# Performance work log

Measured on AMD Instinct MI355X. Metric: run time of the kernel, lower is better.

The kernel has to match this reference:

```python
import jax, jax.numpy as jnp
import numpy as np

B = 2
DZ, DY, DX = 10, 200, 176
N_PER = 100000                      # active voxels per batch element
C_IN, C_MID, C_OUT = 64, 32, 64
STRIDE = 8

_OFFS = np.stack(np.meshgrid(np.arange(3), np.arange(3), np.arange(3), indexing='ij'), -1).reshape(27, 3)


def _build_indices():
    rng = np.random.RandomState(0)
    rows = []
    for b in range(B):
        lin = rng.choice(DZ * DY * DX, size=N_PER, replace=False)
        z, y, x = np.unravel_index(lin, (DZ, DY, DX))
        rows.append(np.stack([np.full(N_PER, b), z, y, x], 1))
    return np.concatenate(rows, 0).astype(np.int32)


def _neighbor_maps(indices):
    # spconv-style indice generation (pure integer bookkeeping, done once in numpy)
    N = indices.shape[0]
    OZ, OY, OX = (DZ - 1) // 2 + 1, (DY - 1) // 2 + 1, (DX - 1) // 2 + 1  # k3 s2 p1 output shape
    hi = np.array([OZ, OY, OX])
    hin = np.array([DZ, DY, DX])
    i3 = indices[:, 1:4].astype(np.int64)
    cand = i3[:, None, :] + 1 - _OFFS[None]          # o*stride = i + pad - k
    valid = (cand % 2 == 0).all(-1)
    o3 = cand // 2
    valid &= ((o3 >= 0) & (o3 < hi)).all(-1)
    ob = np.broadcast_to(indices[:, 0:1], (N, 27))
    flat = np.stack([ob[valid], o3[..., 0][valid], o3[..., 1][valid], o3[..., 2][valid]], 1)
    down = np.unique(flat, axis=0).astype(np.int32)  # [M,4] stride-2 conv output coords
    M = down.shape[0]
    in_grid = -np.ones((B, DZ, DY, DX), np.int32)
    in_grid[indices[:, 0], indices[:, 1], indices[:, 2], indices[:, 3]] = np.arange(N)
    dn_grid = -np.ones((B, OZ, OY, OX), np.int32)
    dn_grid[down[:, 0], down[:, 1], down[:, 2], down[:, 3]] = np.arange(M)
    # stride-2 conv: output row m, kernel k <- input at o*2 - 1 + k
    src = down[:, None, 1:4].astype(np.int64) * 2 - 1 + _OFFS[None]
    ok = ((src >= 0) & (src < hin)).all(-1)
    srcc = np.clip(src, 0, hin - 1)
    nbr_down = np.where(ok, in_grid[down[:, 0:1], srcc[..., 0], srcc[..., 1], srcc[..., 2]], -1).astype(np.int32)
    # submanifold 3x3x3 on down coords
    d3 = down[:, None, 1:4].astype(np.int64) + (_OFFS[None] - 1)
    ok2 = ((d3 >= 0) & (d3 < hi)).all(-1)
    d3c = np.clip(d3, 0, hi - 1)
    nbr_sub = np.where(ok2, dn_grid[down[:, 0:1], d3c[..., 0], d3c[..., 1], d3c[..., 2]], -1).astype(np.int32)
    # inverse conv (transposed pairs of the stride-2 conv): input row n, kernel k <- down row at (i+1-k)/2
    o3c = np.clip(o3, 0, hi - 1)
    nbr_inv = np.where(valid, dn_grid[indices[:, 0:1], o3c[..., 0], o3c[..., 1], o3c[..., 2]], -1).astype(np.int32)
    return down, nbr_down, nbr_sub, nbr_inv


def setup_inputs():
    key = jax.random.key(0)
    ks = jax.random.split(key, 12)
    indices = _build_indices()
    down_indices, nbr_down, nbr_sub, nbr_inv = _neighbor_maps(indices)
    N = indices.shape[0]
    w = lambda k, shp: jax.random.normal(k, shp, jnp.float32) * 0.05
    l2r = np.array([[0., -1., 0., 0.], [0., 0., -1., 0.], [1., 0., 0., 0.]], np.float32)  # lidar->rect
    p2 = np.array([[721.54, 0., 609.56, 44.85], [0., 721.54, 172.85, 0.216], [0., 0., 1., 0.0027]], np.float32)
    return {
        'features': jax.random.normal(ks[0], (N, C_IN), jnp.float32),
        'W_down1': w(ks[1], (27, C_IN, C_MID)),
        'W_res': w(ks[2], (27, C_IN, C_MID)),
        'W_sub2': w(ks[3], (27, C_MID, C_MID)),
        'W_2d1': w(ks[4], (9, C_MID, C_MID)),
        'W_2d2': w(ks[5], (9, C_MID, C_MID)),
        'W_sub3': w(ks[6], (27, C_MID, C_MID)),
        'W_inv4': w(ks[7], (27, C_MID, C_OUT)),
        'bn32_g': 1.0 + 0.1 * jax.random.normal(ks[8], (7, C_MID), jnp.float32),
        'bn32_b': 0.1 * jax.random.normal(ks[9], (7, C_MID), jnp.float32),
        'bn64_g': 1.0 + 0.1 * jax.random.normal(ks[10], (2, C_OUT), jnp.float32),
        'bn64_b': 0.1 * jax.random.normal(ks[11], (2, C_OUT), jnp.float32),
        'calib_l2r': jnp.asarray(np.tile(l2r, (B, 1, 1))),
        'calib_p2': jnp.asarray(np.tile(p2, (B, 1, 1))),
        'down_indices': jnp.asarray(down_indices),
        'nbr_down': jnp.asarray(nbr_down),
        'nbr_sub': jnp.asarray(nbr_sub),
        'nbr_inv': jnp.asarray(nbr_inv),
        'stride': STRIDE,
        'batch_size': B,
    }


def _bn(x, g, b, eps=1e-3):
    # BatchNorm1d training-mode forward (batch stats, biased variance, eps=1e-3)
    m = x.mean(0)
    v = x.var(0)
    return (x - m) * jax.lax.rsqrt(v + eps) * g + b


def _gconv(feats, nbr, W):
    # spconv gather -> GEMM -> accumulate; nbr[m,k] is source row or -1
    out = jnp.zeros((nbr.shape[0], W.shape[-1]), feats.dtype)
    for k in range(W.shape[0]):
        idx = nbr[:, k]
        m = (idx >= 0).astype(feats.dtype)[:, None]
        out = out + (feats[jnp.maximum(idx, 0)] * m) @ W[k]
    return out


def _index2uv(down_indices, calib_l2r, calib_p2, stride):
    vs = 0.05 * stride
    fi = down_indices.astype(jnp.float32)
    x = fi[:, 3] * vs + (0.0 + vs / 2)
    y = fi[:, 2] * vs + (-40.0 + vs / 2)
    z = fi[:, 1] * vs + (-3.0 + vs / 2)
    pts = jnp.stack([x, y, z, jnp.ones_like(x)], 1)           # [M,4] homogeneous lidar pts
    b = down_indices[:, 0]
    rect = jnp.einsum('mi,mji->mj', pts, calib_l2r[b])        # lidar_to_rect
    rh = jnp.concatenate([rect, jnp.ones_like(rect[:, :1])], 1)
    proj = jnp.einsum('mi,mji->mj', rh, calib_p2[b])          # rect_to_img
    u = jax.lax.stop_gradient(proj[:, 0] / proj[:, 2]).astype(jnp.int32)
    v = jax.lax.stop_gradient(proj[:, 1] / proj[:, 2]).astype(jnp.int32)
    u = jnp.clip(u, 0, 1400 - stride) // stride
    v = jnp.clip(v, 0, 400 - stride) // stride
    return b, u, v


def reference(features, W_down1, W_res, W_sub2, W_2d1, W_2d2, W_sub3, W_inv4,
              bn32_g, bn32_b, bn64_g, bn64_b, calib_l2r, calib_p2,
              down_indices, nbr_down, nbr_sub, nbr_inv, stride, batch_size):
    relu = jax.nn.relu
    d3 = relu(_bn(_gconv(features, nbr_down, W_down1), bn32_g[0], bn32_b[0]))   # d3_conv1 (spconv s2)
    d3 = relu(_bn(_gconv(d3, nbr_sub, W_sub2), bn32_g[1], bn32_b[1]))           # d3_conv2 (subm)
    res = relu(_bn(_gconv(features, nbr_down, W_res), bn32_g[2], bn32_b[2]))    # resnet_layer (spconv s2)
    d3 = d3 + res
    # 3D -> 2D reprojection (index2uv) and 2D submanifold conv stage
    b, u, v = _index2uv(down_indices, calib_l2r, calib_p2, stride)
    U, V = 1400 // stride, 400 // stride
    M = d3.shape[0]
    grid = -jnp.ones((batch_size, U, V), jnp.int32)
    grid = grid.at[b, u, v].max(jnp.arange(M, dtype=jnp.int32))  # deterministic dedupe of uv collisions
    du = jnp.repeat(jnp.arange(-1, 2), 3)
    dv = jnp.tile(jnp.arange(-1, 2), 3)
    uu = u[:, None] + du[None]
    vv = v[:, None] + dv[None]
    ok = (uu >= 0) & (uu < U) & (vv >= 0) & (vv < V)
    nbr2d = jnp.where(ok, grid[b[:, None], jnp.clip(uu, 0, U - 1), jnp.clip(vv, 0, V - 1)], -1)
    d2 = relu(_bn(_gconv(d3, nbr2d, W_2d1), bn32_g[3], bn32_b[3]))              # d2_conv1
    d2 = relu(_bn(_gconv(d2, nbr2d, W_2d2), bn32_g[4], bn32_b[4]))              # d2_conv2
    d3 = _bn(d3 + d2, bn32_g[5], bn32_b[5])                                     # mid_norm_fn (no relu)
    d3 = relu(_bn(_gconv(d3, nbr_sub, W_sub3), bn32_g[6], bn32_b[6]))           # d3_conv3
    out = relu(_bn(_gconv(d3, nbr_inv, W_inv4), bn64_g[0], bn64_b[0]))          # d3_conv4 (inverse conv)
    out = _bn(out + features, bn64_g[1], bn64_b[1])                             # output_norm_fn
    return out
```

## Files before the change

### kernel.cpp

```cpp
#include <hip/hip_runtime.h>

#define NBANK 64
#define ACC_STRIDE (NBANK * 128)

typedef _Float16 half8 __attribute__((ext_vector_type(8)));
typedef float    fx4   __attribute__((ext_vector_type(4)));

__global__ void init_kernel(float* __restrict__ acc, int accN, _Float16* __restrict__ zrow,
                            int* __restrict__ grid, int gridN)
{
    int i = blockIdx.x * 256 + threadIdx.x;
    if (i < accN) acc[i] = 0.f;
    if (i < 64) ((float*)zrow)[i] = 0.f;
    if (i < gridN) grid[i] = -1;
}

struct WDesc { const float* W; _Float16* H; _Float16* L; int K, CIN, COUT, base; };
struct WArgs { WDesc d[7]; int total; };

__global__ void wsplit_all_kernel(WArgs a)
{
    int t = blockIdx.x * 256 + threadIdx.x;
    if (t >= a.total) return;
    int seg = 0;
    #pragma unroll
    for (int s = 1; s < 7; ++s) if (t >= a.d[s].base) seg = s;
    const WDesc D = a.d[seg];
    int tt   = t - D.base;
    int lane = tt & 63;
    int frag = tt >> 6;
    int NT = D.COUT >> 4, NS = D.CIN >> 5;
    int ct = frag % NT;
    int s2 = (frag / NT) % NS;
    int k  = frag / (NT * NS);
    int col = ct * 16 + (lane & 15);
    int cib = s2 * 32 + ((lane >> 4) << 3);
    half8 vh, vl;
    #pragma unroll
    for (int j = 0; j < 8; ++j) {
        float w = D.W[(size_t)(k * D.CIN + cib + j) * D.COUT + col];
        _Float16 hh = (_Float16)w;
        vh[j] = hh;
        vl[j] = (_Float16)(w - (float)hh);
    }
    *(half8*)(D.H + (size_t)tt * 8) = vh;
    *(half8*)(D.L + (size_t)tt * 8) = vl;
}

__global__ void tof16_kernel(const float* __restrict__ x, _Float16* __restrict__ h, long total)
{
    long base = ((long)blockIdx.x * 256 + threadIdx.x) * 8;
    if (base >= total) return;
    fx4 v0 = *(const fx4*)(x + base);
    fx4 v1 = *(const fx4*)(x + base + 4);
    half8 hh;
    #pragma unroll
    for (int j = 0; j < 4; ++j) { hh[j] = (_Float16)v0[j]; hh[4 + j] = (_Float16)v1[j]; }
    *(half8*)(h + base) = hh;
}

template <int CIN, int COUT, int K, bool DUAL>
__global__ __launch_bounds__(256) void gconv_mfma_kernel(
    const _Float16* __restrict__ fh, const int* __restrict__ nbr,
    const _Float16* __restrict__ Bh1, const _Float16* __restrict__ Bl1,
    const _Float16* __restrict__ Bh2, const _Float16* __restrict__ Bl2,
    const _Float16* __restrict__ zrow,
    float* __restrict__ out1, float* __restrict__ out2,
    float* __restrict__ sAcc1, float* __restrict__ sAcc2, int M)
{
    constexpr int NS   = CIN / 32;
    constexpr int NT   = COUT / 16;
    constexpr int NCH  = K * NS;
    constexpr int W2   = DUAL ? 2 : 1;
    constexpr int NARR = 2 * W2;
    constexpr int SKB  = NARR * NT;
    constexpr int NLD  = SKB / 4;
    constexpr int RT   = DUAL ? 2 : 4;
    constexpr int RPB  = RT * 64;
    static_assert(NCH % 6 == 0 || NCH % 6 == 3, "tail handling assumes NCH%6 in {0,3}");

    __shared__ _Float16 ldsB[2][SKB * 512];

    const int tid  = threadIdx.x;
    const int lane = tid & 63;
    const int wv   = tid >> 6;
    const int g    = lane >> 4;
    const int r    = lane & 15;
    const int mb   = blockIdx.x * RPB + wv * (RT * 16);

    bool ok[RT];
    #pragma unroll
    for (int t = 0; t < RT; ++t) ok[t] = (mb + t * 16 + r) < M;

    fx4 acc1[RT][NT];
    fx4 acc2[DUAL ? RT : 1][DUAL ? NT : 1];
    const fx4 zf = {0.f, 0.f, 0.f, 0.f};
    #pragma unroll
    for (int rt = 0; rt < RT; ++rt)
        #pragma unroll
        for (int ct = 0; ct < NT; ++ct) acc1[rt][ct] = zf;
    if constexpr (DUAL) {
        #pragma unroll
        for (int rt = 0; rt < RT; ++rt)
            #pragma unroll
            for (int ct = 0; ct < NT; ++ct) acc2[rt][ct] = zf;
    }

    fx4   stg[NLD];
    half8 Breg[NT][2][W2];
    half8 A0[RT], A1[RT], A2[RT];
    int   qa[RT], qb[RT], qc[RT];

    auto idxld = [&](int c, int (&q)[RT]) {
        if (c < NCH) {
            const int k = (NS == 2) ? (c >> 1) : c;
            #pragma unroll
            for (int t = 0; t < RT; ++t)
                q[t] = ok[t] ? nbr[(size_t)(mb + t * 16 + r) * K + k] : -1;
        } else {
            #pragma unroll
            for (int t = 0; t < RT; ++t) q[t] = -1;
        }
    };
    auto loadA = [&](half8 (&A)[RT], const int (&q)[RT], int c) {
        const int cb = (NS == 2) ? ((c & 1) * 32) : 0;
        #pragma unroll
        for (int t = 0; t < RT; ++t) {
            const _Float16* p = (q[t] >= 0) ? fh + (size_t)q[t] * CIN : zrow;
            A[t] = *(const half8*)(p + cb + g * 8);
        }
    };
    auto stage_ld = [&](int c) {
        #pragma unroll
        for (int i = 0; i < NLD; ++i) {
            const int o   = tid * 16 + i * 4096;
            const int arr = o / (NT * 1024);
            const int oa  = o % (NT * 1024);
            const _Float16* ap = (arr == 0) ? Bh1 : (arr == 1) ? Bl1
                                : (arr == 2) ? Bh2 : Bl2;
            stg[i] = *(const fx4*)(ap + (size_t)c * (NT * 512) + oa / 2);
        }
    };
    auto stage_wr = [&](int buf) {
        #pragma unroll
        for (int i = 0; i < NLD; ++i)
            *(fx4*)(&ldsB[buf][0] + (tid * 16 + i * 4096) / 2) = stg[i];
    };
    auto loadB = [&](int buf) {
        #pragma unroll
        for (int ct = 0; ct < NT; ++ct)
            #pragma unroll
            for (int hl = 0; hl < 2; ++hl)
                #pragma unroll
                for (int w = 0; w < W2; ++w) {
                    const int arr = w * 2 + hl;
                    Breg[ct][hl][w] = *(const half8*)(&ldsB[buf][0] + (arr * NT + ct) * 512 + lane * 8);
                }
    };
    auto compute = [&](half8 (&A)[RT]) {
        #pragma unroll
        for (int ct = 0; ct < NT; ++ct)
            #pragma unroll
            for (int rt = 0; rt < RT; ++rt) {
                acc1[rt][ct] = __builtin_amdgcn_mfma_f32_16x16x32_f16(A[rt], Breg[ct][0][0], acc1[rt][ct], 0, 0, 0);
                acc1[rt][ct] = __builtin_amdgcn_mfma_f32_16x16x32_f16(A[rt], Breg[ct][1][0], acc1[rt][ct], 0, 0, 0);
                if constexpr (DUAL) {
                    acc2[rt][ct] = __builtin_amdgcn_mfma_f32_16x16x32_f16(A[rt], Breg[ct][0][1], acc2[rt][ct], 0, 0, 0);
                    acc2[rt][ct] = __builtin_amdgcn_mfma_f32_16x16x32_f16(A[rt], Breg[ct][1][1], acc2[rt][ct], 0, 0, 0);
                }
            }
    };
    auto phase = [&](half8 (&Acur)[RT], half8 (&Aload)[RT], const int (&qUse)[RT],
                     int (&qFill)[RT], int c, int rb, int wb) {
        const bool hn = (c + 1 < NCH);
        if (hn) stage_ld(c + 1);
        loadA(Aload, qUse, c + 2);
        idxld(c + 3, qFill);
        __builtin_amdgcn_s_setprio(1);
        loadB(rb);
        compute(Acur);
        __builtin_amdgcn_s_setprio(0);
        if (hn) stage_wr(wb);
        asm volatile("s_waitcnt lgkmcnt(0)" ::: "memory");
        __builtin_amdgcn_s_barrier();
        __builtin_amdgcn_sched_barrier(0);
    };

    idxld(0, qa);
    loadA(A0, qa, 0);
    idxld(1, qb);
    loadA(A1, qb, 1);
    idxld(2, qc);
    stage_ld(0);
    stage_wr(0);
    asm volatile("s_waitcnt lgkmcnt(0)" ::: "memory");
    __builtin_amdgcn_s_barrier();
    __builtin_amdgcn_sched_barrier(0);

    int c = 0;
    for (; c + 6 <= NCH; c += 6) {
        phase(A0, A2, qc, qa, c + 0, 0, 1);
        phase(A1, A0, qa, qb, c + 1, 1, 0);
        phase(A2, A1, qb, qc, c + 2, 0, 1);
        phase(A0, A2, qc, qa, c + 3, 1, 0);
        phase(A1, A0, qa, qb, c + 4, 0, 1);
        phase(A2, A1, qb, qc, c + 5, 1, 0);
    }
    if constexpr (NCH % 6 == 3) {
        phase(A0, A2, qc, qa, c + 0, 0, 1);
        phase(A1, A0, qa, qb, c + 1, 1, 0);
        phase(A2, A1, qb, qc, c + 2, 0, 1);
    }

    #pragma unroll
    for (int rt = 0; rt < RT; ++rt)
        #pragma unroll
        for (int q = 0; q < 4; ++q) {
            const int rw = mb + rt * 16 + g * 4 + q;
            if (rw < M) {
                #pragma unroll
                for (int ct = 0; ct < NT; ++ct) {
                    out1[(size_t)rw * COUT + ct * 16 + r] = acc1[rt][ct][q];
                    if constexpr (DUAL)
                        out2[(size_t)rw * COUT + ct * 16 + r] = acc2[rt][ct][q];
                }
            }
        }

    #pragma unroll
    for (int ct = 0; ct < NT; ++ct) {
        float s1 = 0.f, p1 = 0.f, s2v = 0.f, p2v = 0.f;
        #pragma unroll
        for (int rt = 0; rt < RT; ++rt)
            #pragma unroll
            for (int q = 0; q < 4; ++q) {
                const int rw = mb + rt * 16 + g * 4 + q;
                if (rw < M) {
                    float v = acc1[rt][ct][q];
                    s1 += v; p1 += v * v;
                    if constexpr (DUAL) { float u = acc2[rt][ct][q]; s2v += u; p2v += u * u; }
                }
            }
        s1 += __shfl_xor(s1, 16, 64); s1 += __shfl_xor(s1, 32, 64);
        p1 += __shfl_xor(p1, 16, 64); p1 += __shfl_xor(p1, 32, 64);
        if constexpr (DUAL) {
            s2v += __shfl_xor(s2v, 16, 64); s2v += __shfl_xor(s2v, 32, 64);
            p2v += __shfl_xor(p2v, 16, 64); p2v += __shfl_xor(p2v, 32, 64);
        }
        if (lane < 16) {
            float* a = sAcc1 + ((blockIdx.x * 4 + wv) & (NBANK - 1)) * 128;
            atomicAdd(&a[ct * 16 + lane], s1);
            atomicAdd(&a[64 + ct * 16 + lane], p1);
            if constexpr (DUAL) {
                float* b2 = sAcc2 + ((blockIdx.x * 4 + wv) & (NBANK - 1)) * 128;
                atomicAdd(&b2[ct * 16 + lane], s2v);
                atomicAdd(&b2[64 + ct * 16 + lane], p2v);
            }
        }
    }
}

template <int C>
__global__ void finalize_kernel(const float* __restrict__ acc, const float* __restrict__ g,
                                const float* __restrict__ b, int M, float* __restrict__ sc)
{
    int c = threadIdx.x;
    if (c < C) {
        float s = 0.f, s2 = 0.f;
        #pragma unroll 8
        for (int k = 0; k < NBANK; ++k) {
            s  += acc[k * 128 + c];
            s2 += acc[k * 128 + 64 + c];
        }
        float inv  = 1.f / (float)M;
        float mean = s * inv;
        float var  = s2 * inv - mean * mean;
        float rstd = rsqrtf(var + 1e-3f);
        float scale = g[c] * rstd;
        sc[c]      = scale;
        sc[64 + c] = b[c] - mean * scale;
    }
}

template <int C>
__global__ __launch_bounds__(256) void apply_kernel(
    const float* __restrict__ x, const float* __restrict__ sc,
    const float* __restrict__ addv, float* __restrict__ outf,
    _Float16* __restrict__ outh, float* __restrict__ statAcc, long total, int relu)
{
    __shared__ float shS[64], shS2[64];
    if (statAcc && threadIdx.x < 64) { shS[threadIdx.x] = 0.f; shS2[threadIdx.x] = 0.f; }

    float s[8], s2[8];
    #pragma unroll
    for (int j = 0; j < 8; ++j) { s[j] = 0.f; s2[j] = 0.f; }

    const long start  = ((long)blockIdx.x * 256 + threadIdx.x) * 8;
    const long stride = (long)gridDim.x * 256 * 8;
    const int  c0     = (int)(start & (C - 1));
    float sA[8], sB[8];
    #pragma unroll
    for (int j = 0; j < 8; ++j) { sA[j] = sc[c0 + j]; sB[j] = sc[64 + c0 + j]; }

    for (long base = start; base < total; base += stride) {
        fx4 v0 = *(const fx4*)(x + base);
        fx4 v1 = *(const fx4*)(x + base + 4);
        float v[8] = {v0[0], v0[1], v0[2], v0[3], v1[0], v1[1], v1[2], v1[3]};
        fx4 a0 = {0.f, 0.f, 0.f, 0.f}, a1 = {0.f, 0.f, 0.f, 0.f};
        if (addv) { a0 = *(const fx4*)(addv + base); a1 = *(const fx4*)(addv + base + 4); }
        #pragma unroll
        for (int j = 0; j < 8; ++j) {
            float w = v[j] * sA[j] + sB[j];
            if (relu) w = fmaxf(w, 0.f);
            if (addv) w += (j < 4) ? a0[j] : a1[j - 4];
            v[j] = w;
            s[j] += w; s2[j] += w * w;
        }
        if (outf) {
            *(fx4*)(outf + base)     = fx4{v[0], v[1], v[2], v[3]};
            *(fx4*)(outf + base + 4) = fx4{v[4], v[5], v[6], v[7]};
        }
        if (outh) {
            half8 hh;
            #pragma unroll
            for (int j = 0; j < 8; ++j) hh[j] = (_Float16)v[j];
            *(half8*)(outh + base) = hh;
        }
    }

    if (statAcc) {
        __syncthreads();
        #pragma unroll
        for (int j = 0; j < 8; ++j) {
            atomicAdd(&shS[c0 + j], s[j]);
            atomicAdd(&shS2[c0 + j], s2[j]);
        }
        __syncthreads();
        if (threadIdx.x < C) {
            float* a = statAcc + (blockIdx.x & (NBANK - 1)) * 128;
            atomicAdd(&a[threadIdx.x], shS[threadIdx.x]);
            atomicAdd(&a[64 + threadIdx.x], shS2[threadIdx.x]);
        }
    }
}

__global__ void uv_scatter_kernel(const int* __restrict__ down, const float* __restrict__ l2r,
                                  const float* __restrict__ p2, int M,
                                  int* __restrict__ ub, int* __restrict__ vb,
                                  int* __restrict__ grid)
{
    __shared__ int shCell[256];
    const int m = blockIdx.x * 256 + threadIdx.x;
    int cell = -1;
    if (m < M) {
        int b = down[4 * m];
        float fz = (float)down[4 * m + 1];
        float fy = (float)down[4 * m + 2];
        float fx = (float)down[4 * m + 3];
        const float vs = 0.4f;
        float x = __fadd_rn(__fmul_rn(fx, vs), 0.2f);
        float y = __fadd_rn(__fmul_rn(fy, vs), -39.79999923706054688f);
        float z = __fadd_rn(__fmul_rn(fz, vs), -2.79999995231628418f);
        double xd = (double)x, yd = (double)y, zd = (double)z;
        const float* L = l2r + b * 12;
        double r0 = (double)L[0] * xd + (double)L[1] * yd + (double)L[2]  * zd + (double)L[3];
        double r1 = (double)L[4] * xd + (double)L[5] * yd + (double)L[6]  * zd + (double)L[7];
        double r2 = (double)L[8] * xd + (double)L[9] * yd + (double)L[10] * zd + (double)L[11];
        const float* P = p2 + b * 12;
        double p0 = (double)P[0] * r0 + (double)P[1] * r1 + (double)P[2]  * r2 + (double)P[3];
        double p1 = (double)P[4] * r0 + (double)P[5] * r1 + (double)P[6]  * r2 + (double)P[7];
        double pz = (double)P[8] * r0 + (double)P[9] * r1 + (double)P[10] * r2 + (double)P[11];
        int u = (int)(p0 / pz);
        int v = (int)(p1 / pz);
        u = min(max(u, 0), 1392) >> 3;
        v = min(max(v, 0), 392) >> 3;
        ub[m] = u;
        vb[m] = v;
        cell = (b * 175 + u) * 50 + v;
    }
    shCell[threadIdx.x] = cell;
    __syncthreads();
    if (m < M) {
        const bool last = (threadIdx.x == 255) || (shCell[threadIdx.x + 1] != cell);
        if (last) atomicMax(&grid[cell], m);
    }
}

__global__ void grid_copy_kernel(const int* __restrict__ grid, int* __restrict__ grid2, int n)
{
    int i = blockIdx.x * 256 + threadIdx.x;
    if (i < n) grid2[i] = grid[i];
}

__global__ void nbr2d_kernel(const int* __restrict__ down, const int* __restrict__ ub,
                             const int* __restrict__ vb, const int* __restrict__ grid,
                             int* __restrict__ nb2, int M)
{
    int m = blockIdx.x * 256 + threadIdx.x;
    if (m >= M) return;
    int b = down[4 * m];
    int u = ub[m], v = vb[m];
    #pragma unroll
    for (int j = 0; j < 9; ++j) {
        int uu = u + j / 3 - 1;
        int vv = v + j % 3 - 1;
        int val = -1;
        if (uu >= 0 && uu < 175 && vv >= 0 && vv < 50) val = grid[(b * 175 + uu) * 50 + vv];
        nb2[m * 9 + j] = val;
    }
}

extern "C" void kernel_launch(void* const* d_in, const int* in_sizes, int n_in,
                              void* d_out, int out_size, void* d_ws, size_t ws_size,
                              hipStream_t stream)
{
    const float* feats  = (const float*)d_in[0];
    const float* Wd1    = (const float*)d_in[1];
    const float* Wres   = (const float*)d_in[2];
    const float* Wsub2  = (const float*)d_in[3];
    const float* W2d1   = (const float*)d_in[4];
    const float* W2d2   = (const float*)d_in[5];
    const float* Wsub3  = (const float*)d_in[6];
    const float* Winv4  = (const float*)d_in[7];
    const float* bn32g  = (const float*)d_in[8];
    const float* bn32b  = (const float*)d_in[9];
    const float* bn64g  = (const float*)d_in[10];
    const float* bn64b  = (const float*)d_in[11];
    const float* l2r    = (const float*)d_in[12];
    const float* p2c    = (const float*)d_in[13];
    const int*   down   = (const int*)d_in[14];
    const int*   nbrD   = (const int*)d_in[15];
    const int*   nbrS   = (const int*)d_in[16];
    const int*   nbrI   = (const int*)d_in[17];

    const int N = in_sizes[0] / 64;
    const int M = in_sizes[14] / 4;

    char* ws = (char*)d_ws;
    size_t off = 0;
    auto alloc = [&](size_t bytes) -> void* {
        void* p = ws + off;
        off = (off + bytes + 255) & ~(size_t)255;
        return p;
    };
    float* t0    = (float*)alloc((size_t)M * 32 * 4);
    float* t1    = (float*)alloc((size_t)M * 32 * 4);
    float* t2    = (float*)alloc((size_t)M * 32 * 4);
    int*   ub    = (int*)alloc((size_t)M * 4);
    int*   vb    = (int*)alloc((size_t)M * 4);
    int*   nb2   = (int*)alloc((size_t)M * 9 * 4);
    int*   grid  = (int*)alloc((size_t)2 * 175 * 50 * 4);
    int*   grid2 = (int*)alloc((size_t)2 * 175 * 50 * 4);
    float* acc   = (float*)alloc((size_t)9 * ACC_STRIDE * 4);
    float* sc    = (float*)alloc((size_t)9 * 128 * 4);
    _Float16* zrow = (_Float16*)alloc(128 * 2);
    _Float16* fhh = (_Float16*)alloc((size_t)N * 64 * 2);
    _Float16* t0h = (_Float16*)alloc((size_t)M * 32 * 2);
    _Float16* t1h = (_Float16*)alloc((size_t)M * 32 * 2);
    _Float16* t2h = (_Float16*)alloc((size_t)M * 32 * 2);
    _Float16* wD1h = (_Float16*)alloc((size_t)55296 * 2);
    _Float16* wD1l = (_Float16*)alloc((size_t)55296 * 2);
    _Float16* wReh = (_Float16*)alloc((size_t)55296 * 2);
    _Float16* wRel = (_Float16*)alloc((size_t)55296 * 2);
    _Float16* wS2h = (_Float16*)alloc((size_t)27648 * 2);
    _Float16* wS2l = (_Float16*)alloc((size_t)27648 * 2);
    _Float16* w21h = (_Float16*)alloc((size_t)9216 * 2);
    _Float16* w21l = (_Float16*)alloc((size_t)9216 * 2);
    _Float16* w22h = (_Float16*)alloc((size_t)9216 * 2);
    _Float16* w22l = (_Float16*)alloc((size_t)9216 * 2);
    _Float16* wS3h = (_Float16*)alloc((size_t)27648 * 2);
    _Float16* wS3l = (_Float16*)alloc((size_t)27648 * 2);
    _Float16* wI4h = (_Float16*)alloc((size_t)55296 * 2);
    _Float16* wI4l = (_Float16*)alloc((size_t)55296 * 2);
    float* g0 = (float*)d_out;

    const int accN = 9 * ACC_STRIDE;
    init_kernel<<<(accN + 255) / 256, 256, 0, stream>>>(acc, accN, zrow, grid, 17500);

    WArgs wa;
    auto mkd = [](const float* W, _Float16* H, _Float16* L, int K, int CIN, int COUT, int base) {
        WDesc d; d.W = W; d.H = H; d.L = L; d.K = K; d.CIN = CIN; d.COUT = COUT; d.base = base;
        return d;
    };
    int b0 = 0;
    wa.d[0] = mkd(Wd1,   wD1h, wD1l, 27, 64, 32, b0); b0 += 27 * 64 * 32 / 8;
    wa.d[1] = mkd(Wres,  wReh, wRel, 27, 64, 32, b0); b0 += 27 * 64 * 32 / 8;
    wa.d[2] = mkd(Wsub2, wS2h, wS2l, 27, 32, 32, b0); b0 += 27 * 32 * 32 / 8;
    wa.d[3] = mkd(W2d1,  w21h, w21l,  9, 32, 32, b0); b0 += 9 * 32 * 32 / 8;
    wa.d[4] = mkd(W2d2,  w22h, w22l,  9, 32, 32, b0); b0 += 9 * 32 * 32 / 8;
    wa.d[5] = mkd(Wsub3, wS3h, wS3l, 27, 32, 32, b0); b0 += 27 * 32 * 32 / 8;
    wa.d[6] = mkd(Winv4, wI4h, wI4l, 27, 32, 64, b0); b0 += 27 * 32 * 64 / 8;
    wa.total = b0;
    wsplit_all_kernel<<<(wa.total + 255) / 256, 256, 0, stream>>>(wa);

    const long totF = (long)N * 64;
    tof16_kernel<<<(int)((totF / 8 + 255) / 256), 256, 0, stream>>>(feats, fhh, totF);

    const int  gTd   = (M + 127) / 128;
    const int  gTs   = (M + 255) / 256;
    const int  gTN   = (N + 255) / 256;
    const long tot32 = (long)M * 32;
    const long tot64 = (long)N * 64;
    const int  ab32  = min((int)((tot32 / 8 + 255) / 256), 2560);
    const int  ab64  = min((int)((tot64 / 8 + 255) / 256), 2560);
    const int  gM    = (M + 255) / 256;

    gconv_mfma_kernel<64, 32, 27, true><<<gTd, 256, 0, stream>>>(
        fhh, nbrD, wD1h, wD1l, wReh, wRel, zrow, t0, t1, acc + 0 * ACC_STRIDE, acc + 1 * ACC_STRIDE, M);
    finalize_kernel<32><<<1, 64, 0, stream>>>(acc + 0 * ACC_STRIDE, bn32g + 0 * 32, bn32b + 0 * 32, M, sc + 0 * 128);
    finalize_kernel<32><<<1, 64, 0, stream>>>(acc + 1 * ACC_STRIDE, bn32g + 2 * 32, bn32b + 2 * 32, M, sc + 1 * 128);
    apply_kernel<32><<<ab32, 256, 0, stream>>>(t0, sc + 0 * 128, nullptr, nullptr, t0h, nullptr, tot32, 1);
    apply_kernel<32><<<ab32, 256, 0, stream>>>(t1, sc + 1 * 128, nullptr, t1, nullptr, nullptr, tot32, 1);

    gconv_mfma_kernel<32, 32, 27, false><<<gTs, 256, 0, stream>>>(
        t0h, nbrS, wS2h, wS2l, nullptr, nullptr, zrow, t2, nullptr, acc + 2 * ACC_STRIDE, nullptr, M);
    finalize_kernel<32><<<1, 64, 0, stream>>>(acc + 2 * ACC_STRIDE, bn32g + 1 * 32, bn32b + 1 * 32, M, sc + 2 * 128);
    apply_kernel<32><<<ab32, 256, 0, stream>>>(t2, sc + 2 * 128, t1, t2, t2h, nullptr, tot32, 1);

    uv_scatter_kernel<<<gM, 256, 0, stream>>>(down, l2r, p2c, M, ub, vb, grid);
    grid_copy_kernel<<<(17500 + 255) / 256, 256, 0, stream>>>(grid, grid2, 17500);
    nbr2d_kernel<<<gM, 256, 0, stream>>>(down, ub, vb, grid2, nb2, M);

    gconv_mfma_kernel<32, 32, 9, false><<<gTs, 256, 0, stream>>>(
        t2h, nb2, w21h, w21l, nullptr, nullptr, zrow, t0, nullptr, acc + 3 * ACC_STRIDE, nullptr, M);
    finalize_kernel<32><<<1, 64, 0, stream>>>(acc + 3 * ACC_STRIDE, bn32g + 3 * 32, bn32b + 3 * 32, M, sc + 3 * 128);
    apply_kernel<32><<<ab32, 256, 0, stream>>>(t0, sc + 3 * 128, nullptr, nullptr, t0h, nullptr, tot32, 1);

    gconv_mfma_kernel<32, 32, 9, false><<<gTs, 256, 0, stream>>>(
        t0h, nb2, w22h, w22l, nullptr, nullptr, zrow, t1, nullptr, acc + 4 * ACC_STRIDE, nullptr, M);
    finalize_kernel<32><<<1, 64, 0, stream>>>(acc + 4 * ACC_STRIDE, bn32g + 4 * 32, bn32b + 4 * 32, M, sc + 4 * 128);
    apply_kernel<32><<<ab32, 256, 0, stream>>>(t1, sc + 4 * 128, t2, t1, nullptr, acc + 5 * ACC_STRIDE, tot32, 1);
    finalize_kernel<32><<<1, 64, 0, stream>>>(acc + 5 * ACC_STRIDE, bn32g + 5 * 32, bn32b + 5 * 32, M, sc + 5 * 128);
    apply_kernel<32><<<ab32, 256, 0, stream>>>(t1, sc + 5 * 128, nullptr, nullptr, t1h, nullptr, tot32, 0);

    gconv_mfma_kernel<32, 32, 27, false><<<gTs, 256, 0, stream>>>(
        t1h, nbrS, wS3h, wS3l, nullptr, nullptr, zrow, t0, nullptr, acc + 6 * ACC_STRIDE, nullptr, M);
    finalize_kernel<32><<<1, 64, 0, stream>>>(acc + 6 * ACC_STRIDE, bn32g + 6 * 32, bn32b + 6 * 32, M, sc + 6 * 128);
    apply_kernel<32><<<ab32, 256, 0, stream>>>(t0, sc + 6 * 128, nullptr, nullptr, t0h, nullptr, tot32, 1);

    gconv_mfma_kernel<32, 64, 27, false><<<gTN, 256, 0, stream>>>(
        t0h, nbrI, wI4h, wI4l, nullptr, nullptr, zrow, g0, nullptr, acc + 7 * ACC_STRIDE, nullptr, N);
    finalize_kernel<64><<<1, 64, 0, stream>>>(acc + 7 * ACC_STRIDE, bn64g + 0 * 64, bn64b + 0 * 64, N, sc + 7 * 128);
    apply_kernel<64><<<ab64, 256, 0, stream>>>(g0, sc + 7 * 128, feats, g0, nullptr, acc + 8 * ACC_STRIDE, tot64, 1);
    finalize_kernel<64><<<1, 64, 0, stream>>>(acc + 8 * ACC_STRIDE, bn64g + 1 * 64, bn64b + 1 * 64, N, sc + 8 * 128);
    apply_kernel<64><<<ab64, 256, 0, stream>>>(g0, sc + 8 * 128, nullptr, (float*)d_out, nullptr, nullptr, tot64, 0);
}
```

Baseline: 571.8 us.

## Fuse BN finalize into producer kernels via last-block counter, merge dual apply, shrink row tiles

Removes the separate single-block finalize launches by having the last block of each gconv or stat-producing apply kernel (found through an atomic done counter) reduce the banked statistics and write scale/shift. The two apply passes after the dual conv are merged into one apply2 kernel. RT is fixed at 2 for all gconv variants, doubling the grid for the non-dual convs. This trades launch overhead and per-block work for extra threadfence/atomic cost and more, smaller blocks.

```diff
diff --git a/kernel.cpp b/kernel.cpp
--- a/kernel.cpp
+++ b/kernel.cpp
@@ -7,12 +7,13 @@
 typedef float    fx4   __attribute__((ext_vector_type(4)));
 
 __global__ void init_kernel(float* __restrict__ acc, int accN, _Float16* __restrict__ zrow,
-                            int* __restrict__ grid, int gridN)
+                            int* __restrict__ grid, int gridN, int* __restrict__ done)
 {
     int i = blockIdx.x * 256 + threadIdx.x;
     if (i < accN) acc[i] = 0.f;
     if (i < 64) ((float*)zrow)[i] = 0.f;
     if (i < gridN) grid[i] = -1;
+    if (i < 16) done[i] = 0;
 }
 
 struct WDesc { const float* W; _Float16* H; _Float16* L; int K, CIN, COUT, base; };
@@ -66,7 +67,11 @@
     const _Float16* __restrict__ Bh2, const _Float16* __restrict__ Bl2,
     const _Float16* __restrict__ zrow,
     float* __restrict__ out1, float* __restrict__ out2,
-    float* __restrict__ sAcc1, float* __restrict__ sAcc2, int M)
+    float* __restrict__ sAcc1, float* __restrict__ sAcc2,
+    const float* __restrict__ g1, const float* __restrict__ b1,
+    const float* __restrict__ g2, const float* __restrict__ b2,
+    float* __restrict__ sc1, float* __restrict__ sc2,
+    int* __restrict__ done, int M)
 {
     constexpr int NS   = CIN / 32;
     constexpr int NT   = COUT / 16;
@@ -75,18 +80,18 @@
     constexpr int NARR = 2 * W2;
     constexpr int SKB  = NARR * NT;
     constexpr int NLD  = SKB / 4;
-    constexpr int RT   = DUAL ? 2 : 4;
-    constexpr int RPB  = RT * 64;
+    constexpr int RT   = 2;
     static_assert(NCH % 6 == 0 || NCH % 6 == 3, "tail handling assumes NCH%6 in {0,3}");
 
     __shared__ _Float16 ldsB[2][SKB * 512];
+    __shared__ int shWin;
 
     const int tid  = threadIdx.x;
     const int lane = tid & 63;
     const int wv   = tid >> 6;
     const int g    = lane >> 4;
     const int r    = lane & 15;
-    const int mb   = blockIdx.x * RPB + wv * (RT * 16);
+    const int mb   = blockIdx.x * (RT * 64) + wv * (RT * 16);
 
     bool ok[RT];
     #pragma unroll
@@ -252,33 +257,49 @@
             atomicAdd(&a[ct * 16 + lane], s1);
             atomicAdd(&a[64 + ct * 16 + lane], p1);
             if constexpr (DUAL) {
-                float* b2 = sAcc2 + ((blockIdx.x * 4 + wv) & (NBANK - 1)) * 128;
-                atomicAdd(&b2[ct * 16 + lane], s2v);
-                atomicAdd(&b2[64 + ct * 16 + lane], p2v);
+                float* b2b = sAcc2 + ((blockIdx.x * 4 + wv) & (NBANK - 1)) * 128;
+                atomicAdd(&b2b[ct * 16 + lane], s2v);
+                atomicAdd(&b2b[64 + ct * 16 + lane], p2v);
             }
         }
     }
-}
-
-template <int C>
-__global__ void finalize_kernel(const float* __restrict__ acc, const float* __restrict__ g,
-                                const float* __restrict__ b, int M, float* __restrict__ sc)
-{
-    int c = threadIdx.x;
-    if (c < C) {
-        float s = 0.f, s2 = 0.f;
-        #pragma unroll 8
-        for (int k = 0; k < NBANK; ++k) {
-            s  += acc[k * 128 + c];
-            s2 += acc[k * 128 + 64 + c];
-        }
-        float inv  = 1.f / (float)M;
-        float mean = s * inv;
-        float var  = s2 * inv - mean * mean;
-        float rstd = rsqrtf(var + 1e-3f);
-        float scale = g[c] * rstd;
-        sc[c]      = scale;
-        sc[64 + c] = b[c] - mean * scale;
+
+    __threadfence();
+    if (tid == 0) shWin = (atomicAdd(done, 1) == (int)gridDim.x - 1) ? 1 : 0;
+    __syncthreads();
+    if (shWin) {
+        if (tid < COUT) {
+            float s = 0.f, s2 = 0.f;
+            #pragma unroll 8
+            for (int k2 = 0; k2 < NBANK; ++k2) {
+                s  += sAcc1[k2 * 128 + tid];
+                s2 += sAcc1[k2 * 128 + 64 + tid];
+            }
+            float inv  = 1.f / (float)M;
+            float mean = s * inv;
+            float var  = s2 * inv - mean * mean;
+            float rstd = rsqrtf(var + 1e-3f);
+            float scale = g1[tid] * rstd;
+            sc1[tid]      = scale;
+            sc1[64 + tid] = b1[tid] - mean * scale;
+        }
+        if constexpr (DUAL) {
+            if (tid < 32) {
+                float s = 0.f, s2 = 0.f;
+                #pragma unroll 8
+                for (int k2 = 0; k2 < NBANK; ++k2) {
+                    s  += sAcc2[k2 * 128 + tid];
+                    s2 += sAcc2[k2 * 128 + 64 + tid];
+                }
+                float inv  = 1.f / (float)M;
+                float mean = s * inv;
+                float var  = s2 * inv - mean * mean;
+                float rstd = rsqrtf(var + 1e-3f);
+                float scale = g2[tid] * rstd;
+                sc2[tid]      = scale;
+                sc2[64 + tid] = b2[tid] - mean * scale;
+            }
+        }
     }
 }
 
@@ -286,9 +307,13 @@
 __global__ __launch_bounds__(256) void apply_kernel(
     const float* __restrict__ x, const float* __restrict__ sc,
     const float* __restrict__ addv, float* __restrict__ outf,
-    _Float16* __restrict__ outh, float* __restrict__ statAcc, long total, int relu)
+    _Float16* __restrict__ outh, float* __restrict__ statAcc,
+    const float* __restrict__ gamma, const float* __restrict__ beta,
+    float* __restrict__ scOut, int* __restrict__ done, int Mstat,
+    long total, int relu)
 {
     __shared__ float shS[64], shS2[64];
+    __shared__ int shWin;
     if (statAcc && threadIdx.x < 64) { shS[threadIdx.x] = 0.f; shS2[threadIdx.x] = 0.f; }
 
     float s[8], s2[8];
@@ -341,6 +366,59 @@
             atomicAdd(&a[threadIdx.x], shS[threadIdx.x]);
             atomicAdd(&a[64 + threadIdx.x], shS2[threadIdx.x]);
         }
+        __threadfence();
+        if (threadIdx.x == 0) shWin = (atomicAdd(done, 1) == (int)gridDim.x - 1) ? 1 : 0;
+        __syncthreads();
+        if (shWin && threadIdx.x < C) {
+            float su = 0.f, sq = 0.f;
+            #pragma unroll 8
+            for (int k2 = 0; k2 < NBANK; ++k2) {
+                su += statAcc[k2 * 128 + threadIdx.x];
+                sq += statAcc[k2 * 128 + 64 + threadIdx.x];
+            }
+            float inv  = 1.f / (float)Mstat;
+            float mean = su * inv;
+            float var  = sq * inv - mean * mean;
+            float rstd = rsqrtf(var + 1e-3f);
+            float scale = gamma[threadIdx.x] * rstd;
+            scOut[threadIdx.x]      = scale;
+            scOut[64 + threadIdx.x] = beta[threadIdx.x] - mean * scale;
+        }
+    }
+}
+
+__global__ __launch_bounds__(256) void apply2_kernel(
+    const float* __restrict__ xa, const float* __restrict__ sca, _Float16* __restrict__ outha,
+    const float* __restrict__ xb, const float* __restrict__ scb, float* __restrict__ outfb,
+    long total)
+{
+    const long start  = ((long)blockIdx.x * 256 + threadIdx.x) * 8;
+    const long stride = (long)gridDim.x * 256 * 8;
+    const int  c0     = (int)(start & 31);
+    float sAa[8], sBa[8], sAb[8], sBb[8];
+    #pragma unroll
+    for (int j = 0; j < 8; ++j) {
+        sAa[j] = sca[c0 + j]; sBa[j] = sca[64 + c0 + j];
+        sAb[j] = scb[c0 + j]; sBb[j] = scb[64 + c0 + j];
+    }
+    for (long base = start; base < total; base += stride) {
+        fx4 va0 = *(const fx4*)(xa + base);
+        fx4 va1 = *(const fx4*)(xa + base + 4);
+        fx4 vb0 = *(const fx4*)(xb + base);
+        fx4 vb1 = *(const fx4*)(xb + base + 4);
+        float va[8] = {va0[0], va0[1], va0[2], va0[3], va1[0], va1[1], va1[2], va1[3]};
+        float vb[8] = {vb0[0], vb0[1], vb0[2], vb0[3], vb1[0], vb1[1], vb1[2], vb1[3]};
+        half8 hh;
+        #pragma unroll
+        for (int j = 0; j < 8; ++j) {
+            float wa = fmaxf(va[j] * sAa[j] + sBa[j], 0.f);
+            float wb = fmaxf(vb[j] * sAb[j] + sBb[j], 0.f);
+            hh[j] = (_Float16)wa;
+            vb[j] = wb;
+        }
+        *(half8*)(outha + base) = hh;
+        *(fx4*)(outfb + base)     = fx4{vb[0], vb[1], vb[2], vb[3]};
+        *(fx4*)(outfb + base + 4) = fx4{vb[4], vb[5], vb[6], vb[7]};
     }
 }
 
@@ -453,6 +531,7 @@
     int*   grid2 = (int*)alloc((size_t)2 * 175 * 50 * 4);
     float* acc   = (float*)alloc((size_t)9 * ACC_STRIDE * 4);
     float* sc    = (float*)alloc((size_t)9 * 128 * 4);
+    int*   done  = (int*)alloc(64 * 4);
     _Float16* zrow = (_Float16*)alloc(128 * 2);
     _Float16* fhh = (_Float16*)alloc((size_t)N * 64 * 2);
     _Float16* t0h = (_Float16*)alloc((size_t)M * 32 * 2);
@@ -475,7 +554,7 @@
     float* g0 = (float*)d_out;
 
     const int accN = 9 * ACC_STRIDE;
-    init_kernel<<<(accN + 255) / 256, 256, 0, stream>>>(acc, accN, zrow, grid, 17500);
+    init_kernel<<<(accN + 255) / 256, 256, 0, stream>>>(acc, accN, zrow, grid, 17500, done);
 
     WArgs wa;
     auto mkd = [](const float* W, _Float16* H, _Float16* L, int K, int CIN, int COUT, int base) {
@@ -496,52 +575,66 @@
     const long totF = (long)N * 64;
     tof16_kernel<<<(int)((totF / 8 + 255) / 256), 256, 0, stream>>>(feats, fhh, totF);
 
-    const int  gTd   = (M + 127) / 128;
-    const int  gTs   = (M + 255) / 256;
-    const int  gTN   = (N + 255) / 256;
+    const int  gT    = (M + 127) / 128;
+    const int  gTN   = (N + 127) / 128;
     const long tot32 = (long)M * 32;
     const long tot64 = (long)N * 64;
     const int  ab32  = min((int)((tot32 / 8 + 255) / 256), 2560);
     const int  ab64  = min((int)((tot64 / 8 + 255) / 256), 2560);
     const int  gM    = (M + 255) / 256;
 
-    gconv_mfma_kernel<64, 32, 27, true><<<gTd, 256, 0, stream>>>(
-        fhh, nbrD, wD1h, wD1l, wReh, wRel, zrow, t0, t1, acc + 0 * ACC_STRIDE, acc + 1 * ACC_STRIDE, M);
-    finalize_kernel<32><<<1, 64, 0, stream>>>(acc + 0 * ACC_STRIDE, bn32g + 0 * 32, bn32b + 0 * 32, M, sc + 0 * 128);
-    finalize_kernel<32><<<1, 64, 0, stream>>>(acc + 1 * ACC_STRIDE, bn32g + 2 * 32, bn32b + 2 * 32, M, sc + 1 * 128);
-    apply_kernel<32><<<ab32, 256, 0, stream>>>(t0, sc + 0 * 128, nullptr, nullptr, t0h, nullptr, tot32, 1);
-    apply_kernel<32><<<ab32, 256, 0, stream>>>(t1, sc + 1 * 128, nullptr, t1, nullptr, nullptr, tot32, 1);
-
-    gconv_mfma_kernel<32, 32, 27, false><<<gTs, 256, 0, stream>>>(
-        t0h, nbrS, wS2h, wS2l, nullptr, nullptr, zrow, t2, nullptr, acc + 2 * ACC_STRIDE, nullptr, M);
-    finalize_kernel<32><<<1, 64, 0, stream>>>(acc + 2 * ACC_STRIDE, bn32g + 1 * 32, bn32b + 1 * 32, M, sc + 2 * 128);
-    apply_kernel<32><<<ab32, 256, 0, stream>>>(t2, sc + 2 * 128, t1, t2, t2h, nullptr, tot32, 1);
+    gconv_mfma_kernel<64, 32, 27, true><<<gT, 256, 0, stream>>>(
+        fhh, nbrD, wD1h, wD1l, wReh, wRel, zrow, t0, t1,
+        acc + 0 * ACC_STRIDE, acc + 1 * ACC_STRIDE,
+        bn32g + 0 * 32, bn32b + 0 * 32, bn32g + 2 * 32, bn32b + 2 * 32,
+        sc + 0 * 128, sc + 1 * 128, done + 0, M);
+    apply2_kernel<<<ab32, 256, 0, stream>>>(t0, sc + 0 * 128, t0h, t1, sc + 1 * 128, t1, tot32);
+
+    gconv_mfma_kernel<32, 32, 27, false><<<gT, 256, 0, stream>>>(
+        t0h, nbrS, wS2h, wS2l, nullptr, nullptr, zrow, t2, nullptr,
+        acc + 2 * ACC_STRIDE, nullptr,
+        bn32g + 1 * 32, bn32b + 1 * 32, nullptr, nullptr,
+        sc + 2 * 128, nullptr, done + 1, M);
+    apply_kernel<32><<<ab32, 256, 0, stream>>>(t2, sc + 2 * 128, t1, t2, t2h,
+        nullptr, nullptr, nullptr, nullptr, nullptr, 0, tot32, 1);
 
     uv_scatter_kernel<<<gM, 256, 0, stream>>>(down, l2r, p2c, M, ub, vb, grid);
     grid_copy_kernel<<<(17500 + 255) / 256, 256, 0, stream>>>(grid, grid2, 17500);
     nbr2d_kernel<<<gM, 256, 0, stream>>>(down, ub, vb, grid2, nb2, M);
 
-    gconv_mfma_kernel<32, 32, 9, false><<<gTs, 256, 0, stream>>>(
-        t2h, nb2, w21h, w21l, nullptr, nullptr, zrow, t0, nullptr, acc + 3 * ACC_STRIDE, nullptr, M);
-    finalize_kernel<32><<<1, 64, 0, stream>>>(acc + 3 * ACC_STRIDE, bn32g + 3 * 32, bn32b + 3 * 32, M, sc + 3 * 128);
-    apply_kernel<32><<<ab32, 256, 0, stream>>>(t0, sc + 3 * 128, nullptr, nullptr, t0h, nullptr, tot32, 1);
-
-    gconv_mfma_kernel<32, 32, 9, false><<<gTs, 256, 0, stream>>>(
-        t0h, nb2, w22h, w22l, nullptr, nullptr, zrow, t1, nullptr, acc + 4 * ACC_STRIDE, nullptr, M);
-    finalize_kernel<32><<<1, 64, 0, stream>>>(acc + 4 * ACC_STRIDE, bn32g + 4 * 32, bn32b + 4 * 32, M, sc + 4 * 128);
-    apply_kernel<32><<<ab32, 256, 0, stream>>>(t1, sc + 4 * 128, t2, t1, nullptr, acc + 5 * ACC_STRIDE, tot32, 1);
-    finalize_kernel<32><<<1, 64, 0, stream>>>(acc + 5 * ACC_STRIDE, bn32g + 5 * 32, bn32b + 5 * 32, M, sc + 5 * 128);
-    apply_kernel<32><<<ab32, 256, 0, stream>>>(t1, sc + 5 * 128, nullptr, nullptr, t1h, nullptr, tot32, 0);
-
-    gconv_mfma_kernel<32, 32, 27, false><<<gTs, 256, 0, stream>>>(
-        t1h, nbrS, wS3h, wS3l, nullptr, nullptr, zrow, t0, nullptr, acc + 6 * ACC_STRIDE, nullptr, M);
-    finalize_kernel<32><<<1, 64, 0, stream>>>(acc + 6 * ACC_STRIDE, bn32g + 6 * 32, bn32b + 6 * 32, M, sc + 6 * 128);
-    apply_kernel<32><<<ab32, 256, 0, stream>>>(t0, sc + 6 * 128, nullptr, nullptr, t0h, nullptr, tot32, 1);
+    gconv_mfma_kernel<32, 32, 9, false><<<gT, 256, 0, stream>>>(
+        t2h, nb2, w21h, w21l, nullptr, nullptr, zrow, t0, nullptr,
+        acc + 3 * ACC_STRIDE, nullptr,
+        bn32g + 3 * 32, bn32b + 3 * 32, nullptr, nullptr,
+        sc + 3 * 128, nullptr, done + 2, M);
+    apply_kernel<32><<<ab32, 256, 0, stream>>>(t0, sc + 3 * 128, nullptr, nullptr, t0h,
+        nullptr, nullptr, nullptr, nullptr, nullptr, 0, tot32, 1);
+
+    gconv_mfma_kernel<32, 32, 9, false><<<gT, 256, 0, stream>>>(
+        t0h, nb2, w22h, w22l, nullptr, nullptr, zrow, t1, nullptr,
+        acc + 4 * ACC_STRIDE, nullptr,
+        bn32g + 4 * 32, bn32b + 4 * 32, nullptr, nullptr,
+        sc + 4 * 128, nullptr, done + 3, M);
+    apply_kernel<32><<<ab32, 256, 0, stream>>>(t1, sc + 4 * 128, t2, t1, nullptr,
+        acc + 5 * ACC_STRIDE, bn32g + 5 * 32, bn32b + 5 * 32, sc + 5 * 128, done + 4, M, tot32, 1);
+    apply_kernel<32><<<ab32, 256, 0, stream>>>(t1, sc + 5 * 128, nullptr, nullptr, t1h,
+        nullptr, nullptr, nullptr, nullptr, nullptr, 0, tot32, 0);
+
+    gconv_mfma_kernel<32, 32, 27, false><<<gT, 256, 0, stream>>>(
+        t1h, nbrS, wS3h, wS3l, nullptr, nullptr, zrow, t0, nullptr,
+        acc + 6 * ACC_STRIDE, nullptr,
+        bn32g + 6 * 32, bn32b + 6 * 32, nullptr, nullptr,
+        sc + 6 * 128, nullptr, done + 5, M);
+    apply_kernel<32><<<ab32, 256, 0, stream>>>(t0, sc + 6 * 128, nullptr, nullptr, t0h,
+        nullptr, nullptr, nullptr, nullptr, nullptr, 0, tot32, 1);
 
     gconv_mfma_kernel<32, 64, 27, false><<<gTN, 256, 0, stream>>>(
-        t0h, nbrI, wI4h, wI4l, nullptr, nullptr, zrow, g0, nullptr, acc + 7 * ACC_STRIDE, nullptr, N);
-    finalize_kernel<64><<<1, 64, 0, stream>>>(acc + 7 * ACC_STRIDE, bn64g + 0 * 64, bn64b + 0 * 64, N, sc + 7 * 128);
-    apply_kernel<64><<<ab64, 256, 0, stream>>>(g0, sc + 7 * 128, feats, g0, nullptr, acc + 8 * ACC_STRIDE, tot64, 1);
-    finalize_kernel<64><<<1, 64, 0, stream>>>(acc + 8 * ACC_STRIDE, bn64g + 1 * 64, bn64b + 1 * 64, N, sc + 8 * 128);
-    apply_kernel<64><<<ab64, 256, 0, stream>>>(g0, sc + 8 * 128, nullptr, (float*)d_out, nullptr, nullptr, tot64, 0);
-}
+        t0h, nbrI, wI4h, wI4l, nullptr, nullptr, zrow, g0, nullptr,
+        acc + 7 * ACC_STRIDE, nullptr,
+        bn64g + 0 * 64, bn64b + 0 * 64, nullptr, nullptr,
+        sc + 7 * 128, nullptr, done + 6, N);
+    apply_kernel<64><<<ab64, 256, 0, stream>>>(g0, sc + 7 * 128, feats, g0, nullptr,
+        acc + 8 * ACC_STRIDE, bn64g + 1 * 64, bn64b + 1 * 64, sc + 8 * 128, done + 7, N, tot64, 1);
+    apply_kernel<64><<<ab64, 256, 0, stream>>>(g0, sc + 8 * 128, nullptr, (float*)d_out, nullptr,
+        nullptr, nullptr, nullptr, nullptr, nullptr, 0, tot64, 0);
+}
```

Measured after the change: 1.424 ms. 2.49x slower.
